# Performance work log

Measured on AMD Instinct MI355X. Metric: run time of the kernel, lower is better.

## Reference

```python
import jax, jax.numpy as jnp
import numpy as np

D_MODEL, D_STATE, EXPAND = 1024, 16, 2
D_INNER = D_MODEL * EXPAND
BATCH, SEQ = 4, 2048
DT = 0.1

def setup_inputs() -> dict:
    key = jax.random.key(0)
    ks = jax.random.split(key, 12)
    s = 0.02
    inp = {
        "x": jax.random.normal(ks[0], (BATCH, SEQ, D_MODEL), jnp.float32),
        "B_mod": jax.random.normal(ks[1], (BATCH, D_STATE), jnp.float32) * 0.1,
        "C_mod": jax.random.normal(ks[2], (BATCH, D_STATE), jnp.float32) * 0.1,
        "W_in": jax.random.normal(ks[3], (D_MODEL, 2 * D_INNER), jnp.float32) * s,
        "b_in": jnp.zeros((2 * D_INNER,), jnp.float32),
        "conv_w": jax.random.normal(ks[4], (D_INNER, 1, 3), jnp.float32) * 0.3,
        "conv_b": jnp.zeros((D_INNER,), jnp.float32),
        "A_log": jnp.tile(jnp.log(jnp.arange(1, D_STATE + 1, dtype=jnp.float32))[None, :], (D_INNER, 1)),
        "D": jnp.ones((D_INNER,), jnp.float32),
        "W_B": jax.random.normal(ks[5], (D_INNER, D_STATE), jnp.float32) * s,
        "b_B": jnp.zeros((D_STATE,), jnp.float32),
        "W_C": jax.random.normal(ks[6], (D_INNER, D_STATE), jnp.float32) * s,
        "b_C": jnp.zeros((D_STATE,), jnp.float32),
        "W_out": jax.random.normal(ks[7], (D_INNER, D_MODEL), jnp.float32) * s,
        "b_out": jnp.zeros((D_MODEL,), jnp.float32),
    }
    return inp

def _silu(v):
    return v * jax.nn.sigmoid(v)

def reference(x, B_mod, C_mod, W_in, b_in, conv_w, conv_b, A_log, D, W_B, b_B, W_C, b_C, W_out, b_out):
    # in_proj + split + gate
    xr = x @ W_in + b_in                      # (B, L, 2*D_INNER)
    x_ssm, x_res = jnp.split(xr, 2, axis=-1)
    x_ssm = _silu(x_ssm)
    # depthwise conv1d, kernel 3, padding 1
    xc = jnp.transpose(x_ssm, (0, 2, 1))      # (B, C, L)
    xc = jax.lax.conv_general_dilated(
        xc, conv_w, window_strides=(1,), padding=[(1, 1)],
        dimension_numbers=("NCH", "OIH", "NCH"), feature_group_count=D_INNER)
    xc = xc + conv_b[None, :, None]
    x_ssm = jnp.transpose(xc, (0, 2, 1))      # (B, L, D_INNER)
    # SSM params
    A = -jnp.exp(A_log)                       # (D_INNER, D_STATE)
    A_bar = jnp.exp(A * DT)
    B = x_ssm @ W_B + b_B + B_mod[:, None, :] # (B, L, D_STATE)
    C = x_ssm @ W_C + b_C + C_mod[:, None, :]
    # sequential scan over time
    def step(h, inp):
        xt, Bt, Ct = inp                      # (B,D_INNER), (B,S), (B,S)
        h = A_bar[None] * h + xt[:, :, None] * Bt[:, None, :]
        yt = jnp.einsum("bds,bs->bd", h, Ct)
        return h, yt
    h0 = jnp.zeros((x.shape[0], D_INNER, D_STATE), x.dtype)
    xs = (jnp.moveaxis(x_ssm, 1, 0), jnp.moveaxis(B, 1, 0), jnp.moveaxis(C, 1, 0))
    _, ys = jax.lax.scan(step, h0, xs)        # (L, B, D_INNER)
    y = jnp.moveaxis(ys, 0, 1) + D[None, None, :] * x_ssm
    y = y * _silu(x_res)
    return y @ W_out + b_out
```

## Files before the change

kernel.cpp:

```cpp
#include <hip/hip_runtime.h>
#include <stdint.h>

#define D_MODEL 1024
#define D_STATE 16
#define D_INNER 2048
#define BATCH   4
#define SEQ     2048
#define ML      (BATCH*SEQ)
#define CH      64
#define NCHUNK  (SEQ/CH)
#define KSEG    8

typedef unsigned short u16;
typedef u16   u16x8  __attribute__((ext_vector_type(8)));
typedef short s16x8  __attribute__((ext_vector_type(8)));
typedef float f32x4  __attribute__((ext_vector_type(4)));

__device__ __forceinline__ float b2f(u16 u){
  union { uint32_t i; float f; } v; v.i = ((uint32_t)u) << 16; return v.f;
}
__device__ __forceinline__ u16 f2b(float f){
  uint32_t x = __float_as_uint(f);
  return (u16)((x + 0x7fffu + ((x >> 16) & 1u)) >> 16);
}
__device__ __forceinline__ float silu_f(float v){
  return v / (1.f + __expf(-v));
}
__device__ __forceinline__ void gl_lds16(const void* gp, void* lp){
  __builtin_amdgcn_global_load_lds(
      (const __attribute__((address_space(1))) void*)gp,
      (__attribute__((address_space(3))) void*)lp, 16, 0, 0);
}

__global__ __launch_bounds__(256) void transpose_cast_k(const float* __restrict__ in,
                                                        u16* __restrict__ out,
                                                        int R, int C){
  __shared__ float tile[32][33];
  int bx = blockIdx.x * 32, by = blockIdx.y * 32;
  int tx = threadIdx.x & 31, ty = threadIdx.x >> 5;
  #pragma unroll
  for (int i = 0; i < 32; i += 8)
    tile[ty + i][tx] = in[(size_t)(by + ty + i) * C + bx + tx];
  __syncthreads();
  #pragma unroll
  for (int i = 0; i < 32; i += 8)
    out[(size_t)(bx + ty + i) * R + by + tx] = f2b(tile[tx][ty + i]);
}

__global__ __launch_bounds__(256) void cast_k(const float* __restrict__ in,
                                              u16* __restrict__ out){
  size_t i = ((size_t)blockIdx.x * 256 + threadIdx.x) * 8;
  f32x4 a = *(const f32x4*)(in + i);
  f32x4 b = *(const f32x4*)(in + i + 4);
  u16x8 o;
  #pragma unroll
  for (int j = 0; j < 4; ++j){ o[j] = f2b(a[j]); o[4+j] = f2b(b[j]); }
  *(u16x8*)(out + i) = o;
}

__global__ __launch_bounds__(256) void bc_wt_k(const float* __restrict__ W_B,
                                               const float* __restrict__ W_C,
                                               u16* __restrict__ Wt){
  int n = blockIdx.y;
  int k = blockIdx.x * 256 + threadIdx.x;
  const float* src = (n < 16) ? W_B : W_C;
  Wt[(size_t)n * D_INNER + k] = f2b(src[(size_t)k * 16 + (n & 15)]);
}

template<int MODE>
__global__ __launch_bounds__(256) void gemm_bt(const u16* __restrict__ A,
                                               const u16* __restrict__ Bt,
                                               const float* __restrict__ bias,
                                               u16* __restrict__ out0,
                                               u16* __restrict__ out1,
                                               float* __restrict__ outf,
                                               int M, int N, int K){
  __shared__ __align__(16) u16 Asb[128*32];
  __shared__ __align__(16) u16 Bsb[128*32];
  const int t    = threadIdx.x;
  const int n0   = blockIdx.x * 128;
  const int m0   = blockIdx.y * 128;
  const int wave = t >> 6, lane = t & 63;
  const int wm   = (wave >> 1) * 64, wn = (wave & 1) * 64;
  const int lrow = lane & 15, kq = (lane >> 4) * 8;
  const int srow = lane >> 2;
  const int scol = (lane & 3) * 8;

  f32x4 acc[4][4];
  #pragma unroll
  for (int i = 0; i < 4; ++i)
    #pragma unroll
    for (int j = 0; j < 4; ++j)
      acc[i][j] = (f32x4){0.f, 0.f, 0.f, 0.f};

  for (int k0 = 0; k0 < K; k0 += 32) {
    #pragma unroll
    for (int i = 0; i < 2; ++i) {
      int R0 = (wave*2 + i) * 16;
      gl_lds16(&A [(size_t)(m0 + R0 + srow)*K + k0 + scol], &Asb[R0*32]);
      gl_lds16(&Bt[(size_t)(n0 + R0 + srow)*K + k0 + scol], &Bsb[R0*32]);
    }
    __syncthreads();
    s16x8 af[4], bfr[4];
    #pragma unroll
    for (int i = 0; i < 4; ++i) af[i]  = *(const s16x8*)&Asb[(wm + i*16 + lrow)*32 + kq];
    #pragma unroll
    for (int j = 0; j < 4; ++j) bfr[j] = *(const s16x8*)&Bsb[(wn + j*16 + lrow)*32 + kq];
    #pragma unroll
    for (int i = 0; i < 4; ++i)
      #pragma unroll
      for (int j = 0; j < 4; ++j)
        acc[i][j] = __builtin_amdgcn_mfma_f32_16x16x32_bf16(af[i], bfr[j], acc[i][j], 0, 0, 0);
    __syncthreads();
  }

  const int Nh = N >> 1;
  #pragma unroll
  for (int i = 0; i < 4; ++i) {
    #pragma unroll
    for (int j = 0; j < 4; ++j) {
      int col = n0 + wn + j*16 + lrow;
      float bv = bias[col];
      #pragma unroll
      for (int r = 0; r < 4; ++r) {
        int row = m0 + wm + i*16 + (lane >> 4)*4 + r;
        float v = acc[i][j][r] + bv;
        if (MODE == 0) {
          outf[(size_t)row * N + col] = v;
        } else {
          float s = silu_f(v);
          if (col < Nh) out0[(size_t)row * Nh + col]        = f2b(s);
          else          out1[(size_t)row * Nh + (col - Nh)] = f2b(s);
        }
      }
    }
  }
}

__global__ __launch_bounds__(256) void conv_k(const u16* __restrict__ xs,
    const float* __restrict__ conv_w, const float* __restrict__ conv_b,
    u16* __restrict__ xconv){
  int bl = blockIdx.x;
  int l = bl & (SEQ-1);
  int d = threadIdx.x * 8;
  const u16* row0 = xs + (size_t)bl * D_INNER + d;

  float f0[8], fm[8], fp[8];
  { u16x8 v = *(const u16x8*)row0;
    #pragma unroll
    for (int j = 0; j < 8; ++j) f0[j] = b2f(v[j]); }
  if (l > 0) {
    u16x8 v = *(const u16x8*)(row0 - D_INNER);
    #pragma unroll
    for (int j = 0; j < 8; ++j) fm[j] = b2f(v[j]);
  } else {
    #pragma unroll
    for (int j = 0; j < 8; ++j) fm[j] = 0.f;
  }
  if (l < SEQ-1) {
    u16x8 v = *(const u16x8*)(row0 + D_INNER);
    #pragma unroll
    for (int j = 0; j < 8; ++j) fp[j] = b2f(v[j]);
  } else {
    #pragma unroll
    for (int j = 0; j < 8; ++j) fp[j] = 0.f;
  }

  const float* wp = conv_w + (size_t)d * 3;
  float wl[24];
  #pragma unroll
  for (int q = 0; q < 6; ++q){
    f32x4 v = *(const f32x4*)(wp + q*4);
    #pragma unroll
    for (int j = 0; j < 4; ++j) wl[q*4 + j] = v[j];
  }
  float cb[8];
  { f32x4 c0 = *(const f32x4*)(conv_b + d), c1 = *(const f32x4*)(conv_b + d + 4);
    #pragma unroll
    for (int j = 0; j < 4; ++j){ cb[j] = c0[j]; cb[4+j] = c1[j]; } }

  u16x8 o;
  #pragma unroll
  for (int j = 0; j < 8; ++j)
    o[j] = f2b(wl[3*j]*fm[j] + wl[3*j+1]*f0[j] + wl[3*j+2]*fp[j] + cb[j]);
  *(u16x8*)(xconv + (size_t)bl * D_INNER + d) = o;
}

__global__ __launch_bounds__(256) void bc_gemm_k(const u16* __restrict__ xconv,
                                                 const u16* __restrict__ Wt,
                                                 float* __restrict__ partial){
  __shared__ __align__(16) u16 Asb[128*40];
  __shared__ __align__(16) u16 Wsb[32*40];
  const int kseg = blockIdx.x;
  const int m0   = blockIdx.y * 128;
  const int t    = threadIdx.x;
  const int wave = t >> 6, lane = t & 63;
  const int wm   = wave * 32;
  const int lrow = lane & 15, kq = (lane >> 4) * 8;

  f32x4 acc[2][2];
  #pragma unroll
  for (int i = 0; i < 2; ++i)
    #pragma unroll
    for (int j = 0; j < 2; ++j)
      acc[i][j] = (f32x4){0.f, 0.f, 0.f, 0.f};

  const int kbase = kseg * (D_INNER / KSEG);
  for (int ks = 0; ks < (D_INNER / KSEG); ks += 32) {
    int k0 = kbase + ks;
    #pragma unroll
    for (int i = 0; i < 2; ++i) {
      int f = (i*256 + t) * 8;
      int r = f >> 5, c = f & 31;
      *(u16x8*)&Asb[r*40 + c] = *(const u16x8*)&xconv[(size_t)(m0 + r)*D_INNER + k0 + c];
    }
    if (t < 128) {
      int f = t * 8;
      int r = f >> 5, c = f & 31;
      *(u16x8*)&Wsb[r*40 + c] = *(const u16x8*)&Wt[(size_t)r*D_INNER + k0 + c];
    }
    __syncthreads();
    s16x8 af[2], wf[2];
    #pragma unroll
    for (int i = 0; i < 2; ++i) af[i] = *(const s16x8*)&Asb[(wm + i*16 + lrow)*40 + kq];
    #pragma unroll
    for (int j = 0; j < 2; ++j) wf[j] = *(const s16x8*)&Wsb[(j*16 + lrow)*40 + kq];
    #pragma unroll
    for (int i = 0; i < 2; ++i)
      #pragma unroll
      for (int j = 0; j < 2; ++j)
        acc[i][j] = __builtin_amdgcn_mfma_f32_16x16x32_bf16(af[i], wf[j], acc[i][j], 0, 0, 0);
    __syncthreads();
  }

  #pragma unroll
  for (int i = 0; i < 2; ++i)
    #pragma unroll
    for (int j = 0; j < 2; ++j)
      #pragma unroll
      for (int r = 0; r < 4; ++r) {
        int row = m0 + wm + i*16 + (lane >> 4)*4 + r;
        int col = j*16 + lrow;
        partial[((size_t)kseg * ML + row) * 32 + col] = acc[i][j][r];
      }
}

__global__ __launch_bounds__(256) void bc_reduce_k(const float* __restrict__ partial,
    const float* __restrict__ b_B, const float* __restrict__ B_mod,
    const float* __restrict__ b_C, const float* __restrict__ C_mod,
    float* __restrict__ Bbuf, float* __restrict__ Cbuf){
  int g = blockIdx.x * 256 + threadIdx.x;
  int row = g >> 5, col = g & 31;
  int b = row >> 11;
  float s = 0.f;
  #pragma unroll
  for (int seg = 0; seg < KSEG; ++seg)
    s += partial[(size_t)seg * ML * 32 + g];
  if (col < 16) Bbuf[(size_t)row*16 + col]      = s + b_B[col]      + B_mod[b*16 + col];
  else          Cbuf[(size_t)row*16 + col - 16] = s + b_C[col - 16] + C_mod[b*16 + col - 16];
}

__global__ __launch_bounds__(256) void state_k(const u16* __restrict__ xconv,
    const float* __restrict__ Bbuf, const float* __restrict__ A_log,
    float* __restrict__ hend){
  int c = blockIdx.x, db = blockIdx.y, b = blockIdx.z;
  int d = db*256 + threadIdx.x;

  float Abar[16];
  #pragma unroll
  for (int s = 0; s < 16; ++s)
    Abar[s] = __expf(-0.1f * __expf(A_log[d*16 + s]));
  float h[16];
  #pragma unroll
  for (int s = 0; s < 16; ++s) h[s] = 0.f;

  size_t base = (size_t)b * SEQ * D_INNER + (size_t)c * CH * D_INNER + d;
  const float* Br = Bbuf + ((size_t)b * SEQ + (size_t)c * CH) * 16;

  float Bc[16];
  #pragma unroll
  for (int s = 0; s < 16; ++s) Bc[s] = Br[s];
  float xn = b2f(xconv[base]);

  for (int l = 0; l < CH; ++l){
    float x = xn;
    float Bl[16];
    #pragma unroll
    for (int s = 0; s < 16; ++s) Bl[s] = Bc[s];
    if (l < CH-1){
      xn = b2f(xconv[base + (size_t)(l+1)*D_INNER]);
      #pragma unroll
      for (int s = 0; s < 16; ++s) Bc[s] = Br[(l+1)*16 + s];
    }
    #pragma unroll
    for (int s = 0; s < 16; ++s)
      h[s] = Abar[s]*h[s] + x*Bl[s];
  }
  float* hp = hend + (((size_t)(b*NCHUNK + c))*D_INNER + d)*16;
  #pragma unroll
  for (int q = 0; q < 4; ++q)
    *(f32x4*)(hp + q*4) = (f32x4){h[q*4], h[q*4+1], h[q*4+2], h[q*4+3]};
}

__global__ __launch_bounds__(256) void prefix_k(const float* __restrict__ hend,
    const float* __restrict__ A_log, float* __restrict__ hin){
  int g = blockIdx.x*256 + threadIdx.x;
  int s = g & 15;
  int d = (g >> 4) & (D_INNER-1);
  int b = g >> 15;
  float decay = __expf(-0.1f * (float)CH * __expf(A_log[d*16 + s]));
  size_t stride = (size_t)D_INNER * 16;
  const float* he = hend + (size_t)b*NCHUNK*stride + (size_t)d*16 + s;
  float*       hi = hin  + (size_t)b*NCHUNK*stride + (size_t)d*16 + s;
  float h = 0.f;
  for (int c0 = 0; c0 < NCHUNK; c0 += 8){
    float v[8];
    #pragma unroll
    for (int i = 0; i < 8; ++i) v[i] = he[(size_t)(c0+i)*stride];
    #pragma unroll
    for (int i = 0; i < 8; ++i){
      hi[(size_t)(c0+i)*stride] = h;
      h = decay*h + v[i];
    }
  }
}

__global__ __launch_bounds__(256) void scan2_k(const u16* __restrict__ xconv,
    const u16* __restrict__ gate, const float* __restrict__ Bbuf, const float* __restrict__ Cbuf,
    const float* __restrict__ A_log, const float* __restrict__ Dp,
    const float* __restrict__ hin, u16* __restrict__ ybuf){
  int c = blockIdx.x, db = blockIdx.y, b = blockIdx.z;
  int d = db*256 + threadIdx.x;

  float Abar[16];
  #pragma unroll
  for (int s = 0; s < 16; ++s)
    Abar[s] = __expf(-0.1f * __expf(A_log[d*16 + s]));
  float h[16];
  const float* hp = hin + (((size_t)(b*NCHUNK + c))*D_INNER + d)*16;
  #pragma unroll
  for (int q = 0; q < 4; ++q){
    f32x4 v = *(const f32x4*)(hp + q*4);
    #pragma unroll
    for (int j = 0; j < 4; ++j) h[q*4 + j] = v[j];
  }
  float Dd = Dp[d];

  size_t base = (size_t)b * SEQ * D_INNER + (size_t)c * CH * D_INNER + d;
  const float* Br = Bbuf + ((size_t)b * SEQ + (size_t)c * CH) * 16;
  const float* Cr = Cbuf + ((size_t)b * SEQ + (size_t)c * CH) * 16;

  float Bc[16], Cc[16];
  #pragma unroll
  for (int s = 0; s < 16; ++s){ Bc[s] = Br[s]; Cc[s] = Cr[s]; }
  float xn = b2f(xconv[base]);
  float gn = b2f(gate[base]);

  for (int l = 0; l < CH; ++l){
    float x = xn, g = gn;
    float Bl[16], Cl[16];
    #pragma unroll
    for (int s = 0; s < 16; ++s){ Bl[s] = Bc[s]; Cl[s] = Cc[s]; }
    if (l < CH-1){
      size_t idx = base + (size_t)(l+1)*D_INNER;
      xn = b2f(xconv[idx]); gn = b2f(gate[idx]);
      #pragma unroll
      for (int s = 0; s < 16; ++s){ Bc[s] = Br[(l+1)*16 + s]; Cc[s] = Cr[(l+1)*16 + s]; }
    }
    float ya[4] = {0.f, 0.f, 0.f, 0.f};
    #pragma unroll
    for (int s = 0; s < 16; ++s){
      float hv = Abar[s]*h[s] + x*Bl[s];
      h[s] = hv;
      ya[s & 3] += hv * Cl[s];
    }
    float y = ((ya[0]+ya[1]) + (ya[2]+ya[3]) + Dd*x) * g;
    ybuf[base + (size_t)l*D_INNER] = f2b(y);
  }
}

extern "C" void kernel_launch(void* const* d_in, const int* in_sizes, int n_in,
                              void* d_out, int out_size, void* d_ws, size_t ws_size,
                              hipStream_t stream){
  const float* x      = (const float*)d_in[0];
  const float* B_mod  = (const float*)d_in[1];
  const float* C_mod  = (const float*)d_in[2];
  const float* W_in   = (const float*)d_in[3];
  const float* b_in   = (const float*)d_in[4];
  const float* conv_w = (const float*)d_in[5];
  const float* conv_b = (const float*)d_in[6];
  const float* A_log  = (const float*)d_in[7];
  const float* Dp     = (const float*)d_in[8];
  const float* W_B    = (const float*)d_in[9];
  const float* b_B    = (const float*)d_in[10];
  const float* W_C    = (const float*)d_in[11];
  const float* b_C    = (const float*)d_in[12];
  const float* W_out  = (const float*)d_in[13];
  const float* b_out  = (const float*)d_in[14];
  float* out = (float*)d_out;

  char* ws = (char*)d_ws;
  size_t off = 0;
  auto alloc = [&](size_t bytes)->char* {
    char* p = ws + off; off += (bytes + 255) & ~(size_t)255; return p;
  };
  u16* Wt_in  = (u16*)alloc((size_t)(2*D_INNER)*D_MODEL*2);
  u16* Wt_out = (u16*)alloc((size_t)D_MODEL*D_INNER*2);
  u16* xs     = (u16*)alloc((size_t)ML*D_INNER*2);
  u16* gatep  = (u16*)alloc((size_t)ML*D_INNER*2);
  u16* xconv  = (u16*)alloc((size_t)ML*D_INNER*2);
  float* Bbuf = (float*)alloc((size_t)ML*D_STATE*4);
  float* Cbuf = (float*)alloc((size_t)ML*D_STATE*4);
  u16* xbf    = (u16*)alloc((size_t)ML*D_MODEL*2);
  float* hin  = (float*)alloc((size_t)BATCH*NCHUNK*D_INNER*16*4);
  u16* Wt_bc  = (u16*)alloc((size_t)32*D_INNER*2);
  float* hend    = (float*)xbf;
  float* partial = (float*)Wt_in;
  u16* ybuf = xs;

  transpose_cast_k<<<dim3((2*D_INNER)/32, D_MODEL/32), 256, 0, stream>>>(W_in, Wt_in, D_MODEL, 2*D_INNER);
  transpose_cast_k<<<dim3(D_MODEL/32, D_INNER/32),     256, 0, stream>>>(W_out, Wt_out, D_INNER, D_MODEL);
  cast_k<<<dim3((ML*D_MODEL)/(256*8)), 256, 0, stream>>>(x, xbf);
  bc_wt_k<<<dim3(D_INNER/256, 32), 256, 0, stream>>>(W_B, W_C, Wt_bc);

  gemm_bt<1><<<dim3((2*D_INNER)/128, ML/128), 256, 0, stream>>>(
      xbf, Wt_in, b_in, xs, gatep, nullptr, ML, 2*D_INNER, D_MODEL);

  conv_k<<<dim3(ML), 256, 0, stream>>>(xs, conv_w, conv_b, xconv);

  bc_gemm_k<<<dim3(KSEG, ML/128), 256, 0, stream>>>(xconv, Wt_bc, partial);
  bc_reduce_k<<<dim3((ML*32)/256), 256, 0, stream>>>(
      partial, b_B, B_mod, b_C, C_mod, Bbuf, Cbuf);

  state_k<<<dim3(NCHUNK, D_INNER/256, BATCH), 256, 0, stream>>>(xconv, Bbuf, A_log, hend);
  prefix_k<<<dim3((BATCH*D_INNER*16)/256), 256, 0, stream>>>(hend, A_log, hin);
  scan2_k<<<dim3(NCHUNK, D_INNER/256, BATCH), 256, 0, stream>>>(
      xconv, gatep, Bbuf, Cbuf, A_log, Dp, hin, ybuf);

  gemm_bt<0><<<dim3(D_MODEL/128, ML/128), 256, 0, stream>>>(
      ybuf, Wt_out, b_out, nullptr, nullptr, out, ML, D_MODEL, D_INNER);
}
```

Before: 400.8 us.

## Double-buffer GEMM LDS tiles and remap blocks for XCD-local N tiles

```diff
diff --git a/kernel.cpp b/kernel.cpp
--- a/kernel.cpp
+++ b/kernel.cpp
@@ -74,12 +74,14 @@
                                                u16* __restrict__ out0,
                                                u16* __restrict__ out1,
                                                float* __restrict__ outf,
-                                               int M, int N, int K){
-  __shared__ __align__(16) u16 Asb[128*32];
-  __shared__ __align__(16) u16 Bsb[128*32];
+                                               int M, int N, int K, int n_per_xcd){
+  __shared__ __align__(16) u16 Asb[2][128*32];
+  __shared__ __align__(16) u16 Bsb[2][128*32];
+  const int bid = blockIdx.x;
+  const int xcd = bid & 7, t2 = bid >> 3;
+  const int n0 = (xcd * n_per_xcd + (t2 % n_per_xcd)) * 128;
+  const int m0 = (t2 / n_per_xcd) * 128;
   const int t    = threadIdx.x;
-  const int n0   = blockIdx.x * 128;
-  const int m0   = blockIdx.y * 128;
   const int wave = t >> 6, lane = t & 63;
   const int wm   = (wave >> 1) * 64, wn = (wave & 1) * 64;
   const int lrow = lane & 15, kq = (lane >> 4) * 8;
@@ -93,19 +95,26 @@
     for (int j = 0; j < 4; ++j)
       acc[i][j] = (f32x4){0.f, 0.f, 0.f, 0.f};
 
-  for (int k0 = 0; k0 < K; k0 += 32) {
+  auto stage = [&](int buf, int k0){
     #pragma unroll
     for (int i = 0; i < 2; ++i) {
       int R0 = (wave*2 + i) * 16;
-      gl_lds16(&A [(size_t)(m0 + R0 + srow)*K + k0 + scol], &Asb[R0*32]);
-      gl_lds16(&Bt[(size_t)(n0 + R0 + srow)*K + k0 + scol], &Bsb[R0*32]);
-    }
-    __syncthreads();
+      gl_lds16(&A [(size_t)(m0 + R0 + srow)*K + k0 + scol], &Asb[buf][R0*32]);
+      gl_lds16(&Bt[(size_t)(n0 + R0 + srow)*K + k0 + scol], &Bsb[buf][R0*32]);
+    }
+  };
+
+  const int KT = K >> 5;
+  stage(0, 0);
+  __syncthreads();
+  for (int kt = 0; kt < KT; ++kt) {
+    const int cur = kt & 1;
+    if (kt + 1 < KT) stage(1 - cur, (kt + 1) * 32);
     s16x8 af[4], bfr[4];
     #pragma unroll
-    for (int i = 0; i < 4; ++i) af[i]  = *(const s16x8*)&Asb[(wm + i*16 + lrow)*32 + kq];
-    #pragma unroll
-    for (int j = 0; j < 4; ++j) bfr[j] = *(const s16x8*)&Bsb[(wn + j*16 + lrow)*32 + kq];
+    for (int i = 0; i < 4; ++i) af[i]  = *(const s16x8*)&Asb[cur][(wm + i*16 + lrow)*32 + kq];
+    #pragma unroll
+    for (int j = 0; j < 4; ++j) bfr[j] = *(const s16x8*)&Bsb[cur][(wn + j*16 + lrow)*32 + kq];
     #pragma unroll
     for (int i = 0; i < 4; ++i)
       #pragma unroll
@@ -423,8 +432,8 @@
   cast_k<<<dim3((ML*D_MODEL)/(256*8)), 256, 0, stream>>>(x, xbf);
   bc_wt_k<<<dim3(D_INNER/256, 32), 256, 0, stream>>>(W_B, W_C, Wt_bc);
 
-  gemm_bt<1><<<dim3((2*D_INNER)/128, ML/128), 256, 0, stream>>>(
-      xbf, Wt_in, b_in, xs, gatep, nullptr, ML, 2*D_INNER, D_MODEL);
+  gemm_bt<1><<<dim3(2048), 256, 0, stream>>>(
+      xbf, Wt_in, b_in, xs, gatep, nullptr, ML, 2*D_INNER, D_MODEL, 4);
 
   conv_k<<<dim3(ML), 256, 0, stream>>>(xs, conv_w, conv_b, xconv);
 
@@ -437,6 +446,6 @@
   scan2_k<<<dim3(NCHUNK, D_INNER/256, BATCH), 256, 0, stream>>>(
       xconv, gatep, Bbuf, Cbuf, A_log, Dp, hin, ybuf);
 
-  gemm_bt<0><<<dim3(D_MODEL/128, ML/128), 256, 0, stream>>>(
-      ybuf, Wt_out, b_out, nullptr, nullptr, out, ML, D_MODEL, D_INNER);
-}
+  gemm_bt<0><<<dim3(512), 256, 0, stream>>>(
+      ybuf, Wt_out, b_out, nullptr, nullptr, out, ML, D_MODEL, D_INNER, 1);
+}
```

New measurement: 387.3 us. -3.4%, faster.
